# Kernel optimization log

Measured on AMD Instinct MI355X. Metric: run time of the kernel, lower is better.

The kernel has to match this reference:

```python
import jax, jax.numpy as jnp
import numpy as np

N_NODES = 100000
N_EDGES = 3200000
D = 64
NUM_RELS = 20
HID_ATTR = 32
OUT_ATTR = 10


def setup_inputs() -> dict:
    key = jax.random.key(0)
    ks = jax.random.split(key, 10)
    h = jax.random.normal(ks[0], (N_NODES, D), dtype=jnp.float32)
    src = jax.random.randint(ks[1], (N_EDGES,), 0, N_NODES)
    dst = jax.random.randint(ks[2], (N_EDGES,), 0, N_NODES)
    etype = jax.random.randint(ks[3], (N_EDGES,), 0, NUM_RELS)
    # RGCN relation weights (num_bases == num_rels, so no basis decomposition)
    s1 = (2.0 / (D + D)) ** 0.5 * (2.0 ** 0.5)  # xavier w/ relu gain, approx
    W1 = jax.random.normal(ks[4], (NUM_RELS, D, D), dtype=jnp.float32) * s1
    W2 = jax.random.normal(ks[5], (NUM_RELS, D, D), dtype=jnp.float32) * s1
    # Attributor MLP params (torch Linear: y = x @ W.T + b; stored here as [in,out])
    A1_w = jax.random.normal(ks[6], (D, HID_ATTR), dtype=jnp.float32) * (1.0 / D ** 0.5)
    A1_b = jnp.zeros((HID_ATTR,), dtype=jnp.float32)
    A2_w = jax.random.normal(ks[7], (HID_ATTR, OUT_ATTR), dtype=jnp.float32) * (1.0 / HID_ATTR ** 0.5)
    A2_b = jnp.zeros((OUT_ATTR,), dtype=jnp.float32)
    return {"h": h, "src": src, "dst": dst, "etype": etype,
            "W1": W1, "W2": W2, "A1_w": A1_w, "A1_b": A1_b,
            "A2_w": A2_w, "A2_b": A2_b}


def _rgcn_layer(h, W, src, dst, etype, activation):
    # Transform all nodes by every relation once (avoids [E,d,d] weight gather),
    # then gather the relation-specific transformed source feature per edge.
    n = h.shape[0]
    t = jnp.einsum('nd,rdo->rno', h, W)          # [R, N, d_out]
    msg = t[etype, src]                           # [E, d_out] irregular gather
    agg = jax.ops.segment_sum(msg, dst, num_segments=n)  # scatter-sum to nodes
    return activation(agg) if activation is not None else agg


def reference(h, src, dst, etype, W1, W2, A1_w, A1_b, A2_w, A2_b):
    # hidden RGCN layer (relu), output RGCN layer (no activation, no bias)
    h1 = _rgcn_layer(h, W1, src, dst, etype, jax.nn.relu)
    h2 = _rgcn_layer(h1, W2, src, dst, etype, None)
    # mean_nodes over the single graph -> [1, D]; Attributor MLP (dropout in eval = identity)
    g = jnp.mean(h2, axis=0, keepdims=True)
    a = jax.nn.relu(g @ A1_w + A1_b)
    a = jax.nn.sigmoid(a @ A2_w + A2_b)
    return (h2, a)
```

## Files before the change

kernel.cpp:

```cpp
#include <hip/hip_runtime.h>
#include <hip/hip_bf16.h>
#include <math.h>
#include <stdint.h>

#define N_NODES 100000
#define N_EDGES 3200000
#define D 64
#define NUM_RELS 20
#define HID_ATTR 32
#define OUT_ATTR 10
#define PADR 72
#define NFB (N_NODES / 16)

#define BUCKET_DSTS 256
#define NB 391
#define PA_THREADS 512
#define PA_EPT 16
#define PA_CHUNK (PA_THREADS * PA_EPT)
#define PA_GRID 391
#define PB_BINS (BUCKET_DSTS * NUM_RELS)

typedef __attribute__((ext_vector_type(8))) short bf16x8;
typedef __attribute__((ext_vector_type(4))) float f32x4;

static __device__ __forceinline__ unsigned short f2bf(float x) {
    unsigned u = __builtin_bit_cast(unsigned, x);
    unsigned r = (u + 0x7FFFu + ((u >> 16) & 1u)) >> 16;
    return (unsigned short)r;
}
static __device__ __forceinline__ float bf2f(unsigned short b) {
    return __builtin_bit_cast(float, (unsigned)b << 16);
}
static __device__ __forceinline__ float bf2f_lo(unsigned u) {
    return __builtin_bit_cast(float, u << 16);
}
static __device__ __forceinline__ float bf2f_hi(unsigned u) {
    return __builtin_bit_cast(float, u & 0xFFFF0000u);
}
static __device__ __forceinline__ unsigned cvt_pk_bf16(float lo, float hi) {
    unsigned r;
    asm("v_cvt_pk_bf16_f32 %0, %1, %2" : "=v"(r) : "v"(lo), "v"(hi));
    return r;
}


__global__ void hist_bucket_kernel(const int* __restrict__ dst, int* __restrict__ hist) {
    __shared__ int h[NB];
    for (int i = threadIdx.x; i < NB; i += PA_THREADS) h[i] = 0;
    __syncthreads();
    int base = blockIdx.x * PA_CHUNK;
#pragma unroll
    for (int k = 0; k < PA_EPT; ++k) {
        int e = base + k * PA_THREADS + threadIdx.x;
        if (e < N_EDGES) atomicAdd(&h[dst[e] >> 8], 1);
    }
    __syncthreads();
    for (int i = threadIdx.x; i < NB; i += PA_THREADS)
        if (h[i]) atomicAdd(&hist[i], h[i]);
}

__global__ void scan_bucket_kernel(const int* __restrict__ hist, int* __restrict__ bbase,
                                   int* __restrict__ bcur, int* __restrict__ sched_off) {
    __shared__ int s[512];
    int t = threadIdx.x;
    int v = (t < NB) ? hist[t] : 0;
    s[t] = v;
    __syncthreads();
    for (int d2 = 1; d2 < 512; d2 <<= 1) {
        int x = (t >= d2) ? s[t - d2] : 0;
        __syncthreads();
        s[t] += x;
        __syncthreads();
    }
    if (t < NB) {
        int b = s[t] - v;
        bbase[t] = b;
        bcur[t] = b;
    }
    if (t == 0) {
        bbase[NB] = N_EDGES;
        sched_off[NFB * 32] = N_EDGES;
    }
}

__global__ __launch_bounds__(PA_THREADS) void passA_kernel(
    const int* __restrict__ src, const int* __restrict__ dst,
    const int* __restrict__ etype, int* __restrict__ bcur,
    unsigned* __restrict__ tmp) {
    __shared__ int h[NB];
    __shared__ int gb[NB];
    __shared__ int c[NB];
    for (int i = threadIdx.x; i < NB; i += PA_THREADS) h[i] = 0;
    __syncthreads();
    int base = blockIdx.x * PA_CHUNK;
    int d[PA_EPT];
#pragma unroll
    for (int k = 0; k < PA_EPT; ++k) {
        int e = base + k * PA_THREADS + threadIdx.x;
        d[k] = (e < N_EDGES) ? dst[e] : -1;
        if (d[k] >= 0) atomicAdd(&h[d[k] >> 8], 1);
    }
    __syncthreads();
    for (int i = threadIdx.x; i < NB; i += PA_THREADS) {
        int n = h[i];
        gb[i] = n ? atomicAdd(&bcur[i], n) : 0;
        c[i] = 0;
    }
    __syncthreads();
#pragma unroll
    for (int k = 0; k < PA_EPT; ++k) {
        int e = base + k * PA_THREADS + threadIdx.x;
        if (d[k] >= 0) {
            int b = d[k] >> 8;
            int sv = src[e], r = etype[e];
            int pos = gb[b] + atomicAdd(&c[b], 1);
            tmp[pos] = ((unsigned)(d[k] & 255) << 22) | ((unsigned)sv << 5) | (unsigned)r;
        }
    }
}

__global__ __launch_bounds__(512) void passB_kernel(
    const unsigned* __restrict__ tmp, const int* __restrict__ bbase,
    unsigned* __restrict__ edgedata, int* __restrict__ sched_off) {
    __shared__ int binpos[PB_BINS];
    __shared__ int blen[PB_BINS];
    __shared__ unsigned sk[16 * 64];
    __shared__ int swo[16 * 64];
    __shared__ int gs[512];
    __shared__ int ssum[512];
    __shared__ int fbb[16];
    int t = threadIdx.x;
    int b = blockIdx.x;
    int beg = bbase[b], end = bbase[b + 1];
    for (int i = t; i < PB_BINS; i += 512) binpos[i] = 0;
    __syncthreads();
    for (int i = beg + t; i < end; i += 512) {
        unsigned v = tmp[i];
        int key = (int)(v >> 22) * NUM_RELS + (int)(v & 31u);
        atomicAdd(&binpos[key], 1);
    }
    __syncthreads();
    for (int i = t; i < PB_BINS; i += 512) blen[i] = binpos[i];
    __syncthreads();
    int loc[10];
    int sum = 0;
#pragma unroll
    for (int j = 0; j < 10; ++j) {
        loc[j] = sum;
        sum += binpos[t * 10 + j];
    }
    ssum[t] = sum;
    __syncthreads();
    for (int d2 = 1; d2 < 512; d2 <<= 1) {
        int x = (t >= d2) ? ssum[t - d2] : 0;
        __syncthreads();
        ssum[t] += x;
        __syncthreads();
    }
    int tbase = beg + ((t > 0) ? ssum[t - 1] : 0);
#pragma unroll
    for (int j = 0; j < 10; ++j) binpos[t * 10 + j] = tbase + loc[j];
    __syncthreads();
    if (t < 16) fbb[t] = binpos[t * 320];
    __syncthreads();
    for (int w = t; w < 1024; w += 512) {
        int fb = w >> 6, wloc = w & 63;
        int nl = wloc >> 2, qt = wloc & 3;
        int b0 = (fb * 16 + nl) * NUM_RELS + qt * 5;
        int len = blen[b0] + blen[b0 + 1] + blen[b0 + 2] + blen[b0 + 3] + blen[b0 + 4];
        sk[fb * 64 + wloc] = ((unsigned)len << 8) | (unsigned)wloc;
    }
    {
        int fb = t >> 5, k = t & 31;
        unsigned* s = &sk[fb * 64];
        for (int size = 2; size <= 64; size <<= 1) {
            for (int stride = size >> 1; stride > 0; stride >>= 1) {
                __syncthreads();
                int i1 = ((k & ~(stride - 1)) << 1) | (k & (stride - 1));
                int i2 = i1 | stride;
                unsigned x = s[i1], y = s[i2];
                bool descb = (i1 & size) == 0;
                if (descb ? (x < y) : (x > y)) { s[i1] = y; s[i2] = x; }
            }
        }
    }
    __syncthreads();
    {
        int fb = t >> 5, k = t & 31;
        unsigned kA = sk[fb * 64 + k], kB = sk[fb * 64 + 63 - k];
        int lenA = (int)(kA >> 8), widA = (int)(kA & 63u);
        int lenB = (int)(kB >> 8), widB = (int)(kB & 63u);
        int tot = lenA + lenB;
        gs[t] = tot;
        __syncthreads();
        for (int d2 = 1; d2 < 32; d2 <<= 1) {
            int x = (k >= d2) ? gs[t - d2] : 0;
            __syncthreads();
            gs[t] += x;
            __syncthreads();
        }
        int gbase = gs[t] - tot;
        swo[fb * 64 + widA] = gbase;
        swo[fb * 64 + widB] = gbase + lenA;
        int gfb = b * 16 + fb;
        if (gfb < NFB) sched_off[gfb * 32 + k] = fbb[fb] + gbase;
    }
    __syncthreads();
    for (int i = t; i < PB_BINS; i += 512) {
        int node = i / 20, rel = i - node * 20;
        int fb = node >> 4, nl = node & 15;
        int qt = rel / 5, rr = rel - qt * 5;
        int wid = nl * 4 + qt;
        int base = fbb[fb] + swo[fb * 64 + wid];
        int b0 = node * 20 + qt * 5;
        for (int r = 0; r < rr; ++r) base += blen[b0 + r];
        binpos[i] = base;
    }
    __syncthreads();
    for (int i = beg + t; i < end; i += 512) {
        unsigned v = tmp[i];
        int dl = (int)(v >> 22), rel = (int)(v & 31u);
        int ro = rel * (16 * PADR) + (dl & 15) * PADR;
        int key = dl * NUM_RELS + rel;
        int pos = atomicAdd(&binpos[key], 1);
        edgedata[pos] = ((v >> 5) & 0x1FFFFu) | ((unsigned)ro << 17);
    }
}


__global__ void f2b_kernel(const float* __restrict__ in, unsigned short* __restrict__ out,
                           int n4) {
    int i = blockIdx.x * 256 + threadIdx.x;
    if (i >= n4) return;
    float4 v = ((const float4*)in)[i];
    ushort4 o;
    o.x = f2bf(v.x); o.y = f2bf(v.y); o.z = f2bf(v.z); o.w = f2bf(v.w);
    ((ushort4*)out)[i] = o;
}

__global__ void wconv_kernel(const float* __restrict__ W, unsigned short* __restrict__ Wb) {
    int r = blockIdx.x;
    for (int i = threadIdx.x; i < D * D; i += 256) {
        int d2 = i >> 6, o = i & 63;
        Wb[(size_t)r * (D * D) + o * D + d2] = f2bf(W[(size_t)r * (D * D) + d2 * D + o]);
    }
}

__global__ __launch_bounds__(512, 6) void fused_layer(
    const unsigned short* __restrict__ xb, const unsigned short* __restrict__ Wb,
    const unsigned* __restrict__ edgedata, const int* __restrict__ sched_off,
    unsigned short* __restrict__ xbout, float* __restrict__ h2out, int mode) {
    __shared__ __align__(16) unsigned short A[NUM_RELS * 16 * PADR];
    int wave = threadIdx.x >> 6, lane = threadIdx.x & 63;
    int grp = lane >> 4, l4 = lane & 15;
    int gidx = wave * 4 + grp;
    int colb = l4 * 4;

    int beg = sched_off[blockIdx.x * 32 + gidx];
    int end = sched_off[blockIdx.x * 32 + gidx + 1];

    for (int i = threadIdx.x; i < NUM_RELS * 16 * PADR / 8; i += 512)
        ((int4*)A)[i] = (int4){0, 0, 0, 0};

    int cnt = end - beg;
    int nb = (cnt + 3) >> 2;
    int nbmax = max(nb, __shfl_xor(nb, 16));
    nbmax = max(nbmax, __shfl_xor(nbmax, 32));
    int endm1 = end - 1;

    float a0 = 0.f, a1 = 0.f, a2 = 0.f, a3 = 0.f;
    unsigned roprev = 0xFFFFFFFFu;
    unsigned short* Ac = A + (unsigned)colb;

    auto rowload = [&](unsigned ewv) -> uint2 {
        return *(const uint2*)(xb + ((ewv & 0x1FFFFu) << 6) + (unsigned)colb);
    };
    auto proc = [&](const unsigned (&ewc)[4], const uint2 (&xv)[4], int valid) {
#pragma unroll
        for (int j = 0; j < 4; ++j) {
            unsigned ro = ewc[j] >> 17;
            bool real = j < valid;
            unsigned mx = real ? xv[j].x : 0u;
            unsigned my = real ? xv[j].y : 0u;
            bool keep = (ro == roprev);
            a0 = (keep ? a0 : 0.f) + bf2f_lo(mx);
            a1 = (keep ? a1 : 0.f) + bf2f_hi(mx);
            a2 = (keep ? a2 : 0.f) + bf2f_lo(my);
            a3 = (keep ? a3 : 0.f) + bf2f_hi(my);
            uint2 o;
            o.x = cvt_pk_bf16(a0, a1);
            o.y = cvt_pk_bf16(a2, a3);
            *(uint2*)(Ac + ro) = o;
            roprev = ro;
        }
    };

    unsigned e0[4], e1[4], e2[4];
    uint2 v0[4], v1[4];
    if (nb > 0) {
#pragma unroll
        for (int j = 0; j < 4; ++j) e0[j] = edgedata[min(beg + j, endm1)];
    }
    if (nb > 1) {
#pragma unroll
        for (int j = 0; j < 4; ++j) e1[j] = edgedata[min(beg + 4 + j, endm1)];
    }
    if (nb > 2) {
#pragma unroll
        for (int j = 0; j < 4; ++j) e2[j] = edgedata[min(beg + 8 + j, endm1)];
    }
    if (nb > 0) {
#pragma unroll
        for (int j = 0; j < 4; ++j) v0[j] = rowload(e0[j]);
    }
    if (nb > 1) {
#pragma unroll
        for (int j = 0; j < 4; ++j) v1[j] = rowload(e1[j]);
    }
    __builtin_amdgcn_sched_barrier(0);
    __syncthreads();

#define PHASE(GG, EW0, EW2, XV0)                                              \
    {                                                                         \
        int gg = (GG);                                                        \
        if (gg < nbmax) {                                                     \
            unsigned ewc[4];                                                  \
            uint2 xvc[4];                                                     \
            _Pragma("unroll") for (int j = 0; j < 4; ++j) {                   \
                ewc[j] = EW0[j]; xvc[j] = XV0[j];                             \
            }                                                                 \
            if (gg + 3 < nb) {                                                \
                int lb = beg + (gg + 3) * 4;                                  \
                _Pragma("unroll") for (int j = 0; j < 4; ++j)                 \
                    EW0[j] = edgedata[min(lb + j, endm1)];                    \
            }                                                                 \
            if (gg + 2 < nb) {                                                \
                _Pragma("unroll") for (int j = 0; j < 4; ++j)                 \
                    XV0[j] = rowload(EW2[j]);                                 \
            }                                                                 \
            __builtin_amdgcn_sched_barrier(0);                                \
            if (gg < nb) proc(ewc, xvc, cnt - gg * 4);                        \
        }                                                                     \
    }

    for (int g = 0; g < nbmax; g += 6) {
        PHASE(g + 0, e0, e2, v0)
        PHASE(g + 1, e1, e0, v1)
        PHASE(g + 2, e2, e1, v0)
        PHASE(g + 3, e0, e2, v1)
        PHASE(g + 4, e1, e0, v0)
        PHASE(g + 5, e2, e1, v1)
    }
#undef PHASE
    __syncthreads();

    if (wave < 4) {
        int lrow = lane & 15, lhi = lane >> 4;
        f32x4 C = {0.f, 0.f, 0.f, 0.f};
        for (int q = 0; q < NUM_RELS; ++q) {
            const unsigned short* Arow = &A[(q * 16 + lrow) * PADR + lhi * 8];
            bf16x8 aa0 = *(const bf16x8*)(Arow);
            bf16x8 aa1 = *(const bf16x8*)(Arow + 32);
            const unsigned short* wrow = Wb + ((size_t)q << 12)
                                         + (size_t)(wave * 16 + lrow) * D + lhi * 8;
            bf16x8 b0 = *(const bf16x8*)(wrow);
            bf16x8 b1 = *(const bf16x8*)(wrow + 32);
            C = __builtin_amdgcn_mfma_f32_16x16x32_bf16(aa0, b0, C, 0, 0, 0);
            C = __builtin_amdgcn_mfma_f32_16x16x32_bf16(aa1, b1, C, 0, 0, 0);
        }
#pragma unroll
        for (int reg = 0; reg < 4; ++reg) {
            int onode = blockIdx.x * 16 + lhi * 4 + reg;
            int col = wave * 16 + lrow;
            if (mode == 1)
                xbout[(size_t)onode * D + col] = f2bf(fmaxf(C[reg], 0.f));
            else
                h2out[(size_t)onode * D + col] = C[reg];
        }
    }
}


__global__ void colsum_kernel(const float* __restrict__ h2,
                              float* __restrict__ g, int n) {
    __shared__ float s[256];
    int tid = threadIdx.x;
    int col = tid & 63;
    int rowgrp = (blockIdx.x * blockDim.x + tid) >> 6;
    int nrowgrp = (gridDim.x * blockDim.x) >> 6;
    float acc = 0.0f;
    for (int row = rowgrp; row < n; row += nrowgrp)
        acc += h2[(size_t)row * D + col];
    s[tid] = acc;
    __syncthreads();
    if (tid < 64) {
        acc = s[tid] + s[tid + 64] + s[tid + 128] + s[tid + 192];
        atomicAdd(&g[col], acc);
    }
}

__global__ void mlp_kernel(const float* __restrict__ g,
                           const float* __restrict__ A1w,
                           const float* __restrict__ A1b,
                           const float* __restrict__ A2w,
                           const float* __restrict__ A2b,
                           float* __restrict__ out, float invN) {
    __shared__ float a1[HID_ATTR];
    int t = threadIdx.x;
    if (t < HID_ATTR) {
        float acc = A1b[t];
#pragma unroll
        for (int d2 = 0; d2 < D; ++d2)
            acc = fmaf(g[d2] * invN, A1w[d2 * HID_ATTR + t], acc);
        a1[t] = fmaxf(acc, 0.0f);
    }
    __syncthreads();
    if (t < OUT_ATTR) {
        float acc = A2b[t];
#pragma unroll
        for (int j = 0; j < HID_ATTR; ++j)
            acc = fmaf(a1[j], A2w[j * OUT_ATTR + t], acc);
        out[t] = 1.0f / (1.0f + expf(-acc));
    }
}


extern "C" void kernel_launch(void* const* d_in, const int* in_sizes, int n_in,
                              void* d_out, int out_size, void* d_ws, size_t ws_size,
                              hipStream_t stream) {
    const float* h   = (const float*)d_in[0];
    const int* src   = (const int*)d_in[1];
    const int* dst   = (const int*)d_in[2];
    const int* etype = (const int*)d_in[3];
    const float* W1  = (const float*)d_in[4];
    const float* W2  = (const float*)d_in[5];
    const float* A1w = (const float*)d_in[6];
    const float* A1b = (const float*)d_in[7];
    const float* A2w = (const float*)d_in[8];
    const float* A2b = (const float*)d_in[9];

    float* out_h2 = (float*)d_out;
    float* out_a  = out_h2 + (size_t)N_NODES * D;

    int* base       = (int*)d_ws;
    float* gsum     = (float*)base;
    int* hist_b     = base + 64;
    int* bbase      = base + 512;
    int* bcur       = base + 960;
    int* sched_off  = base + 1408;
    unsigned* tmp   = (unsigned*)(base + 201472);
    unsigned* edgedata = (unsigned*)(base + 3401472);
    unsigned short* xb  = (unsigned short*)(base + 6601472);
    unsigned short* xb2 = (unsigned short*)(base + 9801472);
    unsigned short* w1b = (unsigned short*)(base + 13001472);
    unsigned short* w2b = (unsigned short*)(base + 13042432);

    hipMemsetAsync(hist_b, 0, NB * sizeof(int), stream);
    hipMemsetAsync(gsum, 0, 64 * sizeof(float), stream);

    hist_bucket_kernel<<<PA_GRID, PA_THREADS, 0, stream>>>(dst, hist_b);
    scan_bucket_kernel<<<1, 512, 0, stream>>>(hist_b, bbase, bcur, sched_off);
    passA_kernel<<<PA_GRID, PA_THREADS, 0, stream>>>(src, dst, etype, bcur, tmp);
    passB_kernel<<<NB, 512, 0, stream>>>(tmp, bbase, edgedata, sched_off);

    wconv_kernel<<<NUM_RELS, 256, 0, stream>>>(W1, w1b);
    wconv_kernel<<<NUM_RELS, 256, 0, stream>>>(W2, w2b);
    f2b_kernel<<<(N_NODES * D / 4 + 255) / 256, 256, 0, stream>>>(h, xb, N_NODES * D / 4);

    fused_layer<<<NFB, 512, 0, stream>>>(xb, w1b, edgedata, sched_off,
                                         xb2, nullptr, 1);
    fused_layer<<<NFB, 512, 0, stream>>>(xb2, w2b, edgedata, sched_off,
                                         nullptr, out_h2, 2);

    colsum_kernel<<<512, 256, 0, stream>>>(out_h2, gsum, N_NODES);
    mlp_kernel<<<1, 64, 0, stream>>>(gsum, A1w, A1b, A2w, A2b,
                                     out_a, 1.0f / (float)N_NODES);
}
```

Before: 571.3 us.

## Bucket edges per 16-node feature block and sort schedule with wave shuffles

Changes the two-pass edge bucketing from 391 buckets of 256 destinations to 6250 buckets of 16 destinations, one per fused_layer block. passB then launches one small 256-thread block per feature block and replaces the shared-memory bitonic sort and scans with wave shuffles. It also merges the two weight conversion launches into one. The aim is more parallelism and fewer barriers in the preprocessing passes, at the cost of much larger shared histograms and more global atomics in passA and the histogram kernel.

```diff
diff --git a/kernel.cpp b/kernel.cpp
--- a/kernel.cpp
+++ b/kernel.cpp
@@ -12,13 +12,12 @@
 #define PADR 72
 #define NFB (N_NODES / 16)
 
-#define BUCKET_DSTS 256
-#define NB 391
+#define NBKT 6250
 #define PA_THREADS 512
 #define PA_EPT 16
 #define PA_CHUNK (PA_THREADS * PA_EPT)
 #define PA_GRID 391
-#define PB_BINS (BUCKET_DSTS * NUM_RELS)
+#define PB_BINS (16 * NUM_RELS)
 
 typedef __attribute__((ext_vector_type(8))) short bf16x8;
 typedef __attribute__((ext_vector_type(4))) float f32x4;
@@ -45,17 +44,17 @@
 
 
 __global__ void hist_bucket_kernel(const int* __restrict__ dst, int* __restrict__ hist) {
-    __shared__ int h[NB];
-    for (int i = threadIdx.x; i < NB; i += PA_THREADS) h[i] = 0;
+    __shared__ int h[NBKT];
+    for (int i = threadIdx.x; i < NBKT; i += PA_THREADS) h[i] = 0;
     __syncthreads();
     int base = blockIdx.x * PA_CHUNK;
 #pragma unroll
     for (int k = 0; k < PA_EPT; ++k) {
         int e = base + k * PA_THREADS + threadIdx.x;
-        if (e < N_EDGES) atomicAdd(&h[dst[e] >> 8], 1);
-    }
-    __syncthreads();
-    for (int i = threadIdx.x; i < NB; i += PA_THREADS)
+        if (e < N_EDGES) atomicAdd(&h[dst[e] >> 4], 1);
+    }
+    __syncthreads();
+    for (int i = threadIdx.x; i < NBKT; i += PA_THREADS)
         if (h[i]) atomicAdd(&hist[i], h[i]);
 }
 
@@ -63,8 +62,16 @@
                                    int* __restrict__ bcur, int* __restrict__ sched_off) {
     __shared__ int s[512];
     int t = threadIdx.x;
-    int v = (t < NB) ? hist[t] : 0;
-    s[t] = v;
+    int loc[13];
+    int sum = 0;
+    int b0 = t * 13;
+#pragma unroll
+    for (int j = 0; j < 13; ++j) {
+        int b = b0 + j;
+        int v = (b < NBKT) ? hist[b] : 0;
+        loc[j] = sum; sum += v;
+    }
+    s[t] = sum;
     __syncthreads();
     for (int d2 = 1; d2 < 512; d2 <<= 1) {
         int x = (t >= d2) ? s[t - d2] : 0;
@@ -72,13 +79,18 @@
         s[t] += x;
         __syncthreads();
     }
-    if (t < NB) {
-        int b = s[t] - v;
-        bbase[t] = b;
-        bcur[t] = b;
+    int base = (t > 0) ? s[t - 1] : 0;
+#pragma unroll
+    for (int j = 0; j < 13; ++j) {
+        int b = b0 + j;
+        if (b < NBKT) {
+            int bb = base + loc[j];
+            bbase[b] = bb;
+            bcur[b] = bb;
+        }
     }
     if (t == 0) {
-        bbase[NB] = N_EDGES;
+        bbase[NBKT] = N_EDGES;
         sched_off[NFB * 32] = N_EDGES;
     }
 }
@@ -87,10 +99,9 @@
     const int* __restrict__ src, const int* __restrict__ dst,
     const int* __restrict__ etype, int* __restrict__ bcur,
     unsigned* __restrict__ tmp) {
-    __shared__ int h[NB];
-    __shared__ int gb[NB];
-    __shared__ int c[NB];
-    for (int i = threadIdx.x; i < NB; i += PA_THREADS) h[i] = 0;
+    __shared__ int h[NBKT];
+    __shared__ int gb[NBKT];
+    for (int i = threadIdx.x; i < NBKT; i += PA_THREADS) h[i] = 0;
     __syncthreads();
     int base = blockIdx.x * PA_CHUNK;
     int d[PA_EPT];
@@ -98,131 +109,93 @@
     for (int k = 0; k < PA_EPT; ++k) {
         int e = base + k * PA_THREADS + threadIdx.x;
         d[k] = (e < N_EDGES) ? dst[e] : -1;
-        if (d[k] >= 0) atomicAdd(&h[d[k] >> 8], 1);
-    }
-    __syncthreads();
-    for (int i = threadIdx.x; i < NB; i += PA_THREADS) {
+        if (d[k] >= 0) atomicAdd(&h[d[k] >> 4], 1);
+    }
+    __syncthreads();
+    for (int i = threadIdx.x; i < NBKT; i += PA_THREADS) {
         int n = h[i];
         gb[i] = n ? atomicAdd(&bcur[i], n) : 0;
-        c[i] = 0;
+        h[i] = 0;
     }
     __syncthreads();
 #pragma unroll
     for (int k = 0; k < PA_EPT; ++k) {
         int e = base + k * PA_THREADS + threadIdx.x;
         if (d[k] >= 0) {
-            int b = d[k] >> 8;
+            int b = d[k] >> 4;
             int sv = src[e], r = etype[e];
-            int pos = gb[b] + atomicAdd(&c[b], 1);
-            tmp[pos] = ((unsigned)(d[k] & 255) << 22) | ((unsigned)sv << 5) | (unsigned)r;
-        }
-    }
-}
-
-__global__ __launch_bounds__(512) void passB_kernel(
+            int pos = gb[b] + atomicAdd(&h[b], 1);
+            tmp[pos] = ((unsigned)(d[k] & 15) << 22) | ((unsigned)sv << 5) | (unsigned)r;
+        }
+    }
+}
+
+__global__ __launch_bounds__(256) void passB_kernel(
     const unsigned* __restrict__ tmp, const int* __restrict__ bbase,
     unsigned* __restrict__ edgedata, int* __restrict__ sched_off) {
     __shared__ int binpos[PB_BINS];
     __shared__ int blen[PB_BINS];
-    __shared__ unsigned sk[16 * 64];
-    __shared__ int swo[16 * 64];
-    __shared__ int gs[512];
-    __shared__ int ssum[512];
-    __shared__ int fbb[16];
+    __shared__ int swo[64];
     int t = threadIdx.x;
-    int b = blockIdx.x;
-    int beg = bbase[b], end = bbase[b + 1];
-    for (int i = t; i < PB_BINS; i += 512) binpos[i] = 0;
-    __syncthreads();
-    for (int i = beg + t; i < end; i += 512) {
+    int fb = blockIdx.x;
+    int beg = bbase[fb], end = bbase[fb + 1];
+    for (int i = t; i < PB_BINS; i += 256) binpos[i] = 0;
+    __syncthreads();
+    for (int i = beg + t; i < end; i += 256) {
         unsigned v = tmp[i];
-        int key = (int)(v >> 22) * NUM_RELS + (int)(v & 31u);
+        int key = (int)((v >> 22) & 15u) * NUM_RELS + (int)(v & 31u);
         atomicAdd(&binpos[key], 1);
     }
     __syncthreads();
-    for (int i = t; i < PB_BINS; i += 512) blen[i] = binpos[i];
-    __syncthreads();
-    int loc[10];
-    int sum = 0;
-#pragma unroll
-    for (int j = 0; j < 10; ++j) {
-        loc[j] = sum;
-        sum += binpos[t * 10 + j];
-    }
-    ssum[t] = sum;
-    __syncthreads();
-    for (int d2 = 1; d2 < 512; d2 <<= 1) {
-        int x = (t >= d2) ? ssum[t - d2] : 0;
-        __syncthreads();
-        ssum[t] += x;
-        __syncthreads();
-    }
-    int tbase = beg + ((t > 0) ? ssum[t - 1] : 0);
-#pragma unroll
-    for (int j = 0; j < 10; ++j) binpos[t * 10 + j] = tbase + loc[j];
-    __syncthreads();
-    if (t < 16) fbb[t] = binpos[t * 320];
-    __syncthreads();
-    for (int w = t; w < 1024; w += 512) {
-        int fb = w >> 6, wloc = w & 63;
-        int nl = wloc >> 2, qt = wloc & 3;
-        int b0 = (fb * 16 + nl) * NUM_RELS + qt * 5;
+    for (int i = t; i < PB_BINS; i += 256) blen[i] = binpos[i];
+    __syncthreads();
+    if (t < 64) {
+        int nl = t >> 2, qt = t & 3;
+        int b0 = nl * NUM_RELS + qt * 5;
         int len = blen[b0] + blen[b0 + 1] + blen[b0 + 2] + blen[b0 + 3] + blen[b0 + 4];
-        sk[fb * 64 + wloc] = ((unsigned)len << 8) | (unsigned)wloc;
-    }
-    {
-        int fb = t >> 5, k = t & 31;
-        unsigned* s = &sk[fb * 64];
+        unsigned key = ((unsigned)len << 8) | (unsigned)t;
         for (int size = 2; size <= 64; size <<= 1) {
             for (int stride = size >> 1; stride > 0; stride >>= 1) {
-                __syncthreads();
-                int i1 = ((k & ~(stride - 1)) << 1) | (k & (stride - 1));
-                int i2 = i1 | stride;
-                unsigned x = s[i1], y = s[i2];
-                bool descb = (i1 & size) == 0;
-                if (descb ? (x < y) : (x > y)) { s[i1] = y; s[i2] = x; }
+                unsigned other = __shfl_xor(key, stride);
+                bool lower = (t & stride) == 0;
+                bool dir = (t & size) == 0;
+                unsigned mx = key > other ? key : other;
+                unsigned mn = key > other ? other : key;
+                key = (lower == dir) ? mx : mn;
             }
         }
-    }
-    __syncthreads();
-    {
-        int fb = t >> 5, k = t & 31;
-        unsigned kA = sk[fb * 64 + k], kB = sk[fb * 64 + 63 - k];
-        int lenA = (int)(kA >> 8), widA = (int)(kA & 63u);
+        unsigned kB = __shfl_xor(key, 63);
+        int lenA = (int)(key >> 8), widA = (int)(key & 63u);
         int lenB = (int)(kB >> 8), widB = (int)(kB & 63u);
         int tot = lenA + lenB;
-        gs[t] = tot;
-        __syncthreads();
-        for (int d2 = 1; d2 < 32; d2 <<= 1) {
-            int x = (k >= d2) ? gs[t - d2] : 0;
-            __syncthreads();
-            gs[t] += x;
-            __syncthreads();
-        }
-        int gbase = gs[t] - tot;
-        swo[fb * 64 + widA] = gbase;
-        swo[fb * 64 + widB] = gbase + lenA;
-        int gfb = b * 16 + fb;
-        if (gfb < NFB) sched_off[gfb * 32 + k] = fbb[fb] + gbase;
-    }
-    __syncthreads();
-    for (int i = t; i < PB_BINS; i += 512) {
-        int node = i / 20, rel = i - node * 20;
-        int fb = node >> 4, nl = node & 15;
+        int sc = tot;
+        for (int off = 1; off < 32; off <<= 1) {
+            int n = __shfl_up(sc, off);
+            if ((t & 31) >= off) sc += n;
+        }
+        if (t < 32) {
+            int gbase = sc - tot;
+            swo[widA] = gbase;
+            swo[widB] = gbase + lenA;
+            sched_off[fb * 32 + t] = beg + gbase;
+        }
+    }
+    __syncthreads();
+    for (int i = t; i < PB_BINS; i += 256) {
+        int nl = i / 20, rel = i - nl * 20;
         int qt = rel / 5, rr = rel - qt * 5;
-        int wid = nl * 4 + qt;
-        int base = fbb[fb] + swo[fb * 64 + wid];
-        int b0 = node * 20 + qt * 5;
+        int b0 = nl * 20 + qt * 5;
+        int base = swo[nl * 4 + qt];
         for (int r = 0; r < rr; ++r) base += blen[b0 + r];
-        binpos[i] = base;
-    }
-    __syncthreads();
-    for (int i = beg + t; i < end; i += 512) {
+        binpos[i] = beg + base;
+    }
+    __syncthreads();
+    for (int i = beg + t; i < end; i += 256) {
         unsigned v = tmp[i];
-        int dl = (int)(v >> 22), rel = (int)(v & 31u);
-        int ro = rel * (16 * PADR) + (dl & 15) * PADR;
-        int key = dl * NUM_RELS + rel;
+        int nl = (int)((v >> 22) & 15u), rel = (int)(v & 31u);
+        int key = nl * 20 + rel;
         int pos = atomicAdd(&binpos[key], 1);
+        int ro = rel * (16 * PADR) + nl * PADR;
         edgedata[pos] = ((v >> 5) & 0x1FFFFu) | ((unsigned)ro << 17);
     }
 }
@@ -238,11 +211,17 @@
     ((ushort4*)out)[i] = o;
 }
 
-__global__ void wconv_kernel(const float* __restrict__ W, unsigned short* __restrict__ Wb) {
+__global__ void wconv_kernel(const float* __restrict__ W1, const float* __restrict__ W2,
+                             unsigned short* __restrict__ w1b,
+                             unsigned short* __restrict__ w2b) {
     int r = blockIdx.x;
+    const float* Ws = (r < NUM_RELS) ? W1 + (size_t)r * (D * D)
+                                     : W2 + (size_t)(r - NUM_RELS) * (D * D);
+    unsigned short* Wd = (r < NUM_RELS) ? w1b + (size_t)r * (D * D)
+                                        : w2b + (size_t)(r - NUM_RELS) * (D * D);
     for (int i = threadIdx.x; i < D * D; i += 256) {
         int d2 = i >> 6, o = i & 63;
-        Wb[(size_t)r * (D * D) + o * D + d2] = f2bf(W[(size_t)r * (D * D) + d2 * D + o]);
+        Wd[o * D + d2] = f2bf(Ws[d2 * D + o]);
     }
 }
 
@@ -445,26 +424,25 @@
     int* base       = (int*)d_ws;
     float* gsum     = (float*)base;
     int* hist_b     = base + 64;
-    int* bbase      = base + 512;
-    int* bcur       = base + 960;
-    int* sched_off  = base + 1408;
-    unsigned* tmp   = (unsigned*)(base + 201472);
-    unsigned* edgedata = (unsigned*)(base + 3401472);
-    unsigned short* xb  = (unsigned short*)(base + 6601472);
-    unsigned short* xb2 = (unsigned short*)(base + 9801472);
-    unsigned short* w1b = (unsigned short*)(base + 13001472);
-    unsigned short* w2b = (unsigned short*)(base + 13042432);
-
-    hipMemsetAsync(hist_b, 0, NB * sizeof(int), stream);
+    int* bbase      = base + 6336;
+    int* bcur       = base + 12608;
+    int* sched_off  = base + 18880;
+    unsigned* tmp   = (unsigned*)(base + 219008);
+    unsigned* edgedata = (unsigned*)(base + 3419008);
+    unsigned short* xb  = (unsigned short*)(base + 6619008);
+    unsigned short* xb2 = (unsigned short*)(base + 9819008);
+    unsigned short* w1b = (unsigned short*)(base + 13019008);
+    unsigned short* w2b = (unsigned short*)(base + 13059968);
+
+    hipMemsetAsync(hist_b, 0, NBKT * sizeof(int), stream);
     hipMemsetAsync(gsum, 0, 64 * sizeof(float), stream);
 
     hist_bucket_kernel<<<PA_GRID, PA_THREADS, 0, stream>>>(dst, hist_b);
     scan_bucket_kernel<<<1, 512, 0, stream>>>(hist_b, bbase, bcur, sched_off);
     passA_kernel<<<PA_GRID, PA_THREADS, 0, stream>>>(src, dst, etype, bcur, tmp);
-    passB_kernel<<<NB, 512, 0, stream>>>(tmp, bbase, edgedata, sched_off);
-
-    wconv_kernel<<<NUM_RELS, 256, 0, stream>>>(W1, w1b);
-    wconv_kernel<<<NUM_RELS, 256, 0, stream>>>(W2, w2b);
+    passB_kernel<<<NBKT, 256, 0, stream>>>(tmp, bbase, edgedata, sched_off);
+
+    wconv_kernel<<<2 * NUM_RELS, 256, 0, stream>>>(W1, W2, w1b, w2b);
     f2b_kernel<<<(N_NODES * D / 4 + 255) / 256, 256, 0, stream>>>(h, xb, N_NODES * D / 4);
 
     fused_layer<<<NFB, 512, 0, stream>>>(xb, w1b, edgedata, sched_off,
```

After: 600.2 us. 5.1% more time.

## Merge prep kernels and fuse column-sum plus MLP into second layer

Applied to the files above, without the earlier changes.

Combines histogram, feature bf16 conversion and weight conversion into one prep launch. Folds the mean-over-nodes reduction into the second fused_layer epilogue, accumulating per-column partials into 32 slices with atomics. The last block to finish, detected with an atomic ticket counter, runs the attributor MLP. This drops several launches and a full re-read of h2, at the cost of extra atomics and a serialized tail in one block.

```diff
diff --git a/kernel.cpp b/kernel.cpp
--- a/kernel.cpp
+++ b/kernel.cpp
@@ -20,6 +20,10 @@
 #define PA_GRID 391
 #define PB_BINS (BUCKET_DSTS * NUM_RELS)
 
+#define F2B_BLOCKS 3125
+#define WC_BLOCKS (2 * NUM_RELS)
+#define PREP_GRID (NB + F2B_BLOCKS + WC_BLOCKS)
+
 typedef __attribute__((ext_vector_type(8))) short bf16x8;
 typedef __attribute__((ext_vector_type(4))) float f32x4;
 
@@ -28,9 +32,6 @@
     unsigned r = (u + 0x7FFFu + ((u >> 16) & 1u)) >> 16;
     return (unsigned short)r;
 }
-static __device__ __forceinline__ float bf2f(unsigned short b) {
-    return __builtin_bit_cast(float, (unsigned)b << 16);
-}
 static __device__ __forceinline__ float bf2f_lo(unsigned u) {
     return __builtin_bit_cast(float, u << 16);
 }
@@ -43,26 +44,50 @@
     return r;
 }
 
-
-__global__ void hist_bucket_kernel(const int* __restrict__ dst, int* __restrict__ hist) {
-    __shared__ int h[NB];
-    for (int i = threadIdx.x; i < NB; i += PA_THREADS) h[i] = 0;
-    __syncthreads();
-    int base = blockIdx.x * PA_CHUNK;
-#pragma unroll
-    for (int k = 0; k < PA_EPT; ++k) {
-        int e = base + k * PA_THREADS + threadIdx.x;
-        if (e < N_EDGES) atomicAdd(&h[dst[e] >> 8], 1);
-    }
-    __syncthreads();
-    for (int i = threadIdx.x; i < NB; i += PA_THREADS)
-        if (h[i]) atomicAdd(&hist[i], h[i]);
+__global__ __launch_bounds__(512) void prep_kernel(
+    const int* __restrict__ dst, int* __restrict__ hist,
+    const float* __restrict__ hin, unsigned short* __restrict__ xb,
+    const float* __restrict__ W1, const float* __restrict__ W2,
+    unsigned short* __restrict__ w1b, unsigned short* __restrict__ w2b) {
+    int bid = blockIdx.x;
+    if (bid < NB) {
+        __shared__ int h[NB];
+        for (int i = threadIdx.x; i < NB; i += 512) h[i] = 0;
+        __syncthreads();
+        int base = bid * PA_CHUNK;
+#pragma unroll
+        for (int k = 0; k < PA_EPT; ++k) {
+            int e = base + k * 512 + threadIdx.x;
+            if (e < N_EDGES) atomicAdd(&h[dst[e] >> 8], 1);
+        }
+        __syncthreads();
+        for (int i = threadIdx.x; i < NB; i += 512)
+            if (h[i]) atomicAdd(&hist[i], h[i]);
+    } else if (bid < NB + F2B_BLOCKS) {
+        int i = (bid - NB) * 512 + threadIdx.x;
+        float4 v = ((const float4*)hin)[i];
+        ushort4 o;
+        o.x = f2bf(v.x); o.y = f2bf(v.y); o.z = f2bf(v.z); o.w = f2bf(v.w);
+        ((ushort4*)xb)[i] = o;
+    } else {
+        int r = bid - (NB + F2B_BLOCKS);
+        const float* Ws = (r < NUM_RELS) ? W1 + (size_t)r * (D * D)
+                                         : W2 + (size_t)(r - NUM_RELS) * (D * D);
+        unsigned short* Wd = (r < NUM_RELS) ? w1b + (size_t)r * (D * D)
+                                            : w2b + (size_t)(r - NUM_RELS) * (D * D);
+        for (int i = threadIdx.x; i < D * D; i += 512) {
+            int d2 = i >> 6, o = i & 63;
+            Wd[o * D + d2] = f2bf(Ws[d2 * D + o]);
+        }
+    }
 }
 
 __global__ void scan_bucket_kernel(const int* __restrict__ hist, int* __restrict__ bbase,
-                                   int* __restrict__ bcur, int* __restrict__ sched_off) {
+                                   int* __restrict__ bcur, int* __restrict__ sched_off,
+                                   int* __restrict__ gpart_i) {
     __shared__ int s[512];
     int t = threadIdx.x;
+    for (int i = t; i < 2049; i += 512) gpart_i[i] = 0;
     int v = (t < NB) ? hist[t] : 0;
     s[t] = v;
     __syncthreads();
@@ -227,29 +252,14 @@
     }
 }
 
-
-__global__ void f2b_kernel(const float* __restrict__ in, unsigned short* __restrict__ out,
-                           int n4) {
-    int i = blockIdx.x * 256 + threadIdx.x;
-    if (i >= n4) return;
-    float4 v = ((const float4*)in)[i];
-    ushort4 o;
-    o.x = f2bf(v.x); o.y = f2bf(v.y); o.z = f2bf(v.z); o.w = f2bf(v.w);
-    ((ushort4*)out)[i] = o;
-}
-
-__global__ void wconv_kernel(const float* __restrict__ W, unsigned short* __restrict__ Wb) {
-    int r = blockIdx.x;
-    for (int i = threadIdx.x; i < D * D; i += 256) {
-        int d2 = i >> 6, o = i & 63;
-        Wb[(size_t)r * (D * D) + o * D + d2] = f2bf(W[(size_t)r * (D * D) + d2 * D + o]);
-    }
-}
-
 __global__ __launch_bounds__(512, 6) void fused_layer(
     const unsigned short* __restrict__ xb, const unsigned short* __restrict__ Wb,
     const unsigned* __restrict__ edgedata, const int* __restrict__ sched_off,
-    unsigned short* __restrict__ xbout, float* __restrict__ h2out, int mode) {
+    unsigned short* __restrict__ xbout, float* __restrict__ h2out, int mode,
+    float* __restrict__ gpart, int* __restrict__ done_ctr,
+    const float* __restrict__ A1w, const float* __restrict__ A1b,
+    const float* __restrict__ A2w, const float* __restrict__ A2b,
+    float* __restrict__ out_a, float invN) {
     __shared__ __align__(16) unsigned short A[NUM_RELS * 16 * PADR];
     int wave = threadIdx.x >> 6, lane = threadIdx.x & 63;
     int grp = lane >> 4, l4 = lane & 15;
@@ -377,50 +387,52 @@
             else
                 h2out[(size_t)onode * D + col] = C[reg];
         }
-    }
-}
-
-
-__global__ void colsum_kernel(const float* __restrict__ h2,
-                              float* __restrict__ g, int n) {
-    __shared__ float s[256];
-    int tid = threadIdx.x;
-    int col = tid & 63;
-    int rowgrp = (blockIdx.x * blockDim.x + tid) >> 6;
-    int nrowgrp = (gridDim.x * blockDim.x) >> 6;
-    float acc = 0.0f;
-    for (int row = rowgrp; row < n; row += nrowgrp)
-        acc += h2[(size_t)row * D + col];
-    s[tid] = acc;
-    __syncthreads();
-    if (tid < 64) {
-        acc = s[tid] + s[tid + 64] + s[tid + 128] + s[tid + 192];
-        atomicAdd(&g[col], acc);
-    }
-}
-
-__global__ void mlp_kernel(const float* __restrict__ g,
-                           const float* __restrict__ A1w,
-                           const float* __restrict__ A1b,
-                           const float* __restrict__ A2w,
-                           const float* __restrict__ A2b,
-                           float* __restrict__ out, float invN) {
-    __shared__ float a1[HID_ATTR];
-    int t = threadIdx.x;
-    if (t < HID_ATTR) {
-        float acc = A1b[t];
-#pragma unroll
-        for (int d2 = 0; d2 < D; ++d2)
-            acc = fmaf(g[d2] * invN, A1w[d2 * HID_ATTR + t], acc);
-        a1[t] = fmaxf(acc, 0.0f);
-    }
-    __syncthreads();
-    if (t < OUT_ATTR) {
-        float acc = A2b[t];
-#pragma unroll
-        for (int j = 0; j < HID_ATTR; ++j)
-            acc = fmaf(a1[j], A2w[j * OUT_ATTR + t], acc);
-        out[t] = 1.0f / (1.0f + expf(-acc));
+        if (mode == 2) {
+            float s = C[0] + C[1] + C[2] + C[3];
+            s += __shfl_xor(s, 16);
+            s += __shfl_xor(s, 32);
+            if (lane < 16) {
+                int col = wave * 16 + lane;
+                atomicAdd(&gpart[(blockIdx.x & 31) * 64 + col], s);
+            }
+        }
+    }
+
+    if (mode == 2) {
+        __threadfence();
+        __shared__ int lastflag;
+        __syncthreads();
+        if (threadIdx.x == 0) {
+            int tkt = atomicAdd(done_ctr, 1);
+            lastflag = (tkt == NFB - 1) ? 1 : 0;
+        }
+        __syncthreads();
+        if (lastflag) {
+            __shared__ float sg[D];
+            __shared__ float a1s[HID_ATTR];
+            if (threadIdx.x < D) {
+                float s = 0.f;
+                for (int sl = 0; sl < 32; ++sl)
+                    s += atomicAdd(&gpart[sl * 64 + threadIdx.x], 0.0f);
+                sg[threadIdx.x] = s;
+            }
+            __syncthreads();
+            if (threadIdx.x < HID_ATTR) {
+                float acc = A1b[threadIdx.x];
+#pragma unroll
+                for (int d2 = 0; d2 < D; ++d2)
+                    acc = fmaf(sg[d2] * invN, A1w[d2 * HID_ATTR + threadIdx.x], acc);
+                a1s[threadIdx.x] = fmaxf(acc, 0.0f);
+            }
+            __syncthreads();
+            if (threadIdx.x < OUT_ATTR) {
+                float acc = A2b[threadIdx.x];
+#pragma unroll
+                for (int j = 0; j < HID_ATTR; ++j)
+                    acc = fmaf(a1s[j], A2w[j * OUT_ATTR + threadIdx.x], acc);
+                out_a[threadIdx.x] = 1.0f / (1.0f + expf(-acc));
+            }
+        }
     }
 }
 
@@ -443,36 +455,36 @@
     float* out_a  = out_h2 + (size_t)N_NODES * D;
 
     int* base       = (int*)d_ws;
-    float* gsum     = (float*)base;
-    int* hist_b     = base + 64;
-    int* bbase      = base + 512;
-    int* bcur       = base + 960;
-    int* sched_off  = base + 1408;
-    unsigned* tmp   = (unsigned*)(base + 201472);
-    unsigned* edgedata = (unsigned*)(base + 3401472);
-    unsigned short* xb  = (unsigned short*)(base + 6601472);
-    unsigned short* xb2 = (unsigned short*)(base + 9801472);
-    unsigned short* w1b = (unsigned short*)(base + 13001472);
-    unsigned short* w2b = (unsigned short*)(base + 13042432);
+    float* gpart    = (float*)base;
+    int* done_ctr   = base + 2048;
+    int* hist_b     = base + 2112;
+    int* bbase      = base + 2560;
+    int* bcur       = base + 3008;
+    int* sched_off  = base + 3456;
+    unsigned* tmp   = (unsigned*)(base + 203520);
+    unsigned* edgedata = (unsigned*)(base + 3403520);
+    unsigned short* xb  = (unsigned short*)(base + 6603520);
+    unsigned short* xb2 = (unsigned short*)(base + 9803520);
+    unsigned short* w1b = (unsigned short*)(base + 13003520);
+    unsigned short* w2b = (unsigned short*)(base + 13044480);
 
     hipMemsetAsync(hist_b, 0, NB * sizeof(int), stream);
-    hipMemsetAsync(gsum, 0, 64 * sizeof(float), stream);
-
-    hist_bucket_kernel<<<PA_GRID, PA_THREADS, 0, stream>>>(dst, hist_b);
-    scan_bucket_kernel<<<1, 512, 0, stream>>>(hist_b, bbase, bcur, sched_off);
+
+    prep_kernel<<<PREP_GRID, 512, 0, stream>>>(dst, hist_b, h, xb,
+                                               W1, W2, w1b, w2b);
+    scan_bucket_kernel<<<1, 512, 0, stream>>>(hist_b, bbase, bcur, sched_off,
+                                              (int*)gpart);
     passA_kernel<<<PA_GRID, PA_THREADS, 0, stream>>>(src, dst, etype, bcur, tmp);
     passB_kernel<<<NB, 512, 0, stream>>>(tmp, bbase, edgedata, sched_off);
 
-    wconv_kernel<<<NUM_RELS, 256, 0, stream>>>(W1, w1b);
-    wconv_kernel<<<NUM_RELS, 256, 0, stream>>>(W2, w2b);
-    f2b_kernel<<<(N_NODES * D / 4 + 255) / 256, 256, 0, stream>>>(h, xb, N_NODES * D / 4);
-
     fused_layer<<<NFB, 512, 0, stream>>>(xb, w1b, edgedata, sched_off,
-                                         xb2, nullptr, 1);
+                                         xb2, nullptr, 1,
+                                         nullptr, nullptr,
+                                         nullptr, nullptr, nullptr, nullptr,
+                                         nullptr, 0.f);
     fused_layer<<<NFB, 512, 0, stream>>>(xb2, w2b, edgedata, sched_off,
-                                         nullptr, out_h2, 2);
-
-    colsum_kernel<<<512, 256, 0, stream>>>(out_h2, gsum, N_NODES);
-    mlp_kernel<<<1, 64, 0, stream>>>(gsum, A1w, A1b, A2w, A2b,
-                                     out_a, 1.0f / (float)N_NODES);
-}
+                                         nullptr, out_h2, 2,
+                                         gpart, done_ctr,
+                                         A1w, A1b, A2w, A2b,
+                                         out_a, 1.0f / (float)N_NODES);
+}
```

New measurement: 1.822 ms. 3.19x slower.
